# Performance work log

Hardware: AMD Instinct MI355X
Metric: run time of the kernel (lower is better)

## Reference

```python
import jax, jax.numpy as jnp
import numpy as np

B, T, D, H = 1024, 64, 256, 256  # batch, time steps, input_size, hidden_size


def setup_inputs() -> dict:
    key = jax.random.key(0)
    ks = jax.random.split(key, 5)
    s = 0.05
    return {
        "input_data": jax.random.normal(ks[0], (B, T, D), jnp.float32),
        # nn.Linear(2H+T, 1)
        "W_attn": jax.random.normal(ks[1], (1, 2 * H + T), jnp.float32) * s,
        "b_attn": jnp.zeros((1,), jnp.float32),
        # nn.LSTM(input_size=D, hidden_size=H, num_layers=1); gate order i,f,g,o
        "W_ih": jax.random.normal(ks[2], (4 * H, D), jnp.float32) * s,
        "W_hh": jax.random.normal(ks[3], (4 * H, H), jnp.float32) * s,
        "b_ih": jnp.zeros((4 * H,), jnp.float32),
        "b_hh": jnp.zeros((4 * H,), jnp.float32),
    }


def _encoder(input_data, W_attn, b_attn, W_ih, W_hh, b_ih, b_hh):
    Bv, Tv, Dv = input_data.shape
    Hv = W_hh.shape[1]
    # attn_linear applied to concat([h, c, x_series]) decomposes exactly into
    # three dot products (same math, no giant concat materialized each step).
    w_h = W_attn[0, :Hv]            # (H,)  weight on hidden part
    w_c = W_attn[0, Hv:2 * Hv]      # (H,)  weight on cell part
    w_x = W_attn[0, 2 * Hv:]        # (T,)  weight on per-feature time series
    # input_data.permute(0,2,1) @ w_x is constant across steps -> precompute.
    x_score = jnp.einsum('btd,t->bd', input_data, w_x) + b_attn[0]  # (B, D)

    xs = jnp.moveaxis(input_data, 1, 0)  # (T, B, D)

    def step(carry, x_t):
        h, c = carry                              # each (B, H)
        s_hc = h @ w_h + c @ w_c                  # (B,) same across features
        attn = jax.nn.softmax(s_hc[:, None] + x_score, axis=1)  # (B, D)
        w_in = attn * x_t                         # weighted input, (B, D)
        gates = w_in @ W_ih.T + h @ W_hh.T + b_ih + b_hh  # (B, 4H)
        i, f, g, o = jnp.split(gates, 4, axis=1)
        c_new = jax.nn.sigmoid(f) * c + jax.nn.sigmoid(i) * jnp.tanh(g)
        h_new = jax.nn.sigmoid(o) * jnp.tanh(c_new)
        return (h_new, c_new), (w_in, h_new)

    h0 = jnp.zeros((Bv, Hv), input_data.dtype)
    c0 = jnp.zeros((Bv, Hv), input_data.dtype)
    _, (ws, hs) = jax.lax.scan(step, (h0, c0), xs)
    input_weighted = jnp.moveaxis(ws, 0, 1)  # (B, T, D)
    input_encoded = jnp.moveaxis(hs, 0, 1)   # (B, T, H)
    return input_weighted, input_encoded


def reference(input_data, W_attn, b_attn, W_ih, W_hh, b_ih, b_hh):
    return _encoder(input_data, W_attn, b_attn, W_ih, W_hh, b_ih, b_hh)
```

## Files before the change

kernel.cpp:

```cpp
#include <hip/hip_runtime.h>
#include <hip/hip_bf16.h>
#include <stdint.h>

#define B_ 1024
#define T_ 64
#define D_ 256
#define H_ 256
#define G_ 1024

typedef float f32x4 __attribute__((ext_vector_type(4)));
typedef __bf16 bf16x8 __attribute__((ext_vector_type(8)));
typedef unsigned int u32x4 __attribute__((ext_vector_type(4)));

#if __has_builtin(__builtin_amdgcn_rcpf)
#define RCP(x) __builtin_amdgcn_rcpf(x)
#else
#define RCP(x) (1.f / (x))
#endif

__device__ __forceinline__ float bf2f(unsigned int u) {
    unsigned int x = u << 16;
    return __builtin_bit_cast(float, x);
}
__device__ __forceinline__ unsigned short f2bf(float f) {
    __hip_bfloat16 h = __float2bfloat16(f);
    return __builtin_bit_cast(unsigned short, h);
}

__global__ void prep_w_kernel(const float* __restrict__ Wih, const float* __restrict__ Whh,
                              const float* __restrict__ bih, const float* __restrict__ bhh,
                              unsigned short* __restrict__ wih_bf, unsigned short* __restrict__ whh_bf,
                              float* __restrict__ bias) {
    int i = blockIdx.x * 256 + threadIdx.x;
    wih_bf[i] = f2bf(Wih[i]);
    whh_bf[i] = f2bf(Whh[i]);
    if (i < G_) bias[i] = bih[i] + bhh[i];
}

__global__ void prep_attn_kernel(const float* __restrict__ x, const float* __restrict__ Wattn,
                                 float* __restrict__ attn) {
    __shared__ float wx[T_];
    __shared__ float red[256];
    int b = blockIdx.x, d = threadIdx.x;
    if (d < T_) wx[d] = Wattn[2 * H_ + d];
    __syncthreads();
    const float* xb = x + (size_t)b * T_ * D_ + d;
    float s = 0.f;
    #pragma unroll
    for (int t = 0; t < T_; ++t) s += xb[t * D_] * wx[t];
    red[d] = s;
    __syncthreads();
    for (int o = 128; o > 0; o >>= 1) {
        if (d < o) red[d] = fmaxf(red[d], red[d + o]);
        __syncthreads();
    }
    float m = red[0];
    __syncthreads();
    float e = __expf(s - m);
    red[d] = e;
    __syncthreads();
    for (int o = 128; o > 0; o >>= 1) {
        if (d < o) red[d] += red[d + o];
        __syncthreads();
    }
    attn[b * D_ + d] = e * (1.f / red[0]);
}

__global__ void winw_kernel(const float* __restrict__ x, const float* __restrict__ attn,
                            float* __restrict__ w_out, unsigned short* __restrict__ win_bf) {
    int i4 = blockIdx.x * 256 + threadIdx.x;
    int e  = i4 * 4;
    int d  = e & 255;
    int bt = e >> 8;
    int b  = bt >> 6, t = bt & 63;
    f32x4 xv = *(const f32x4*)(x + e);
    f32x4 av = *(const f32x4*)(attn + b * D_ + d);
    f32x4 w  = xv * av;
    *(f32x4*)(w_out + e) = w;
    ushort4 u;
    u.x = f2bf(w[0]); u.y = f2bf(w[1]); u.z = f2bf(w[2]); u.w = f2bf(w[3]);
    *(ushort4*)(win_bf + ((size_t)(t * B_ + b) * D_ + d)) = u;
}

__global__ __launch_bounds__(256, 2) void gemmx_kernel(const unsigned short* __restrict__ A,
                                                       const unsigned short* __restrict__ Bw,
                                                       unsigned short* __restrict__ pre) {
    int bx = blockIdx.x;
    int bn = bx & 7, bm = bx >> 3;
    int tid = threadIdx.x, lane = tid & 63, w = tid >> 6;
    int wr = w >> 1, wc = w & 1;
    int m0 = bm * 128 + wr * 64, n0 = bn * 128 + wc * 64;
    int lr = lane & 15, lk = (lane >> 4) * 8;

    const unsigned short* Ab[4];
    const unsigned short* Bb[4];
    #pragma unroll
    for (int i = 0; i < 4; ++i) {
        Ab[i] = A  + (size_t)(m0 + i * 16 + lr) * D_ + lk;
        Bb[i] = Bw + (size_t)(n0 + i * 16 + lr) * D_ + lk;
    }
    f32x4 acc[4][4] = {};
    #pragma unroll
    for (int kk = 0; kk < 8; ++kk) {
        bf16x8 a[4], bb[4];
        #pragma unroll
        for (int i = 0; i < 4; ++i) {
            a[i]  = *(const bf16x8*)(Ab[i] + kk * 32);
            bb[i] = *(const bf16x8*)(Bb[i] + kk * 32);
        }
        #pragma unroll
        for (int mi = 0; mi < 4; ++mi)
            #pragma unroll
            for (int ni = 0; ni < 4; ++ni)
                acc[mi][ni] = __builtin_amdgcn_mfma_f32_16x16x32_bf16(a[mi], bb[ni], acc[mi][ni], 0, 0, 0);
    }
    int orow = (lane >> 4) * 4;
    #pragma unroll
    for (int mi = 0; mi < 4; ++mi)
        #pragma unroll
        for (int ni = 0; ni < 4; ++ni)
            #pragma unroll
            for (int q = 0; q < 4; ++q) {
                int m = m0 + mi * 16 + orow + q;
                int n = n0 + ni * 16 + lr;
                pre[(size_t)m * G_ + n] = f2bf(acc[mi][ni][q]);
            }
}

__global__ __launch_bounds__(512, 2) void seqs_kernel(const unsigned short* __restrict__ pre,
                                                      const unsigned short* __restrict__ Whh,
                                                      const float* __restrict__ bias,
                                                      float* __restrict__ enc_out) {
    extern __shared__ char smem[];
    unsigned short* W_lds    = (unsigned short*)smem;
    unsigned short* h_par    = (unsigned short*)(smem + 135168);
    float*          bias_lds = (float*)(smem + 135168 + 16896);

    int tid = threadIdx.x, lane = tid & 63, w = tid >> 6;
    int lr = lane & 15, hi = lane >> 4;
    int r0 = blockIdx.x * 16;
    int j0 = w * 32;

    for (int i = tid; i < 1024; i += 512) bias_lds[i] = bias[i];
    for (int i = tid; i < 2 * 16 * 264; i += 512) h_par[i] = 0;
    #pragma unroll
    for (int l = 0; l < 2; ++l) {
        int n = l * 256 + j0 + 16 + lr;
        const u32x4* src = (const u32x4*)(Whh + (size_t)n * 256);
        #pragma unroll
        for (int c = 0; c < 8; ++c) {
            int ch = hi + c * 4;
            *(u32x4*)&W_lds[((w * 2 + l) * 16 + lr) * 264 + ch * 8] = src[ch];
        }
    }
    bf16x8 Wreg[4][8];
    #pragma unroll
    for (int g = 0; g < 4; ++g)
        #pragma unroll
        for (int kk = 0; kk < 8; ++kk)
            Wreg[g][kk] = *(const bf16x8*)(Whh + (size_t)(g * 256 + j0 + lr) * 256 + kk * 32 + hi * 8);
    const unsigned short* Ws[2];
    #pragma unroll
    for (int s = 0; s < 2; ++s)
        Ws[s] = Whh + (size_t)((s + 2) * 256 + j0 + 16 + lr) * 256 + hi * 8;
    bf16x8 sbuf[2][4];
    #pragma unroll
    for (int s = 0; s < 2; ++s)
        #pragma unroll
        for (int k2 = 0; k2 < 4; ++k2)
            sbuf[s][k2] = *(const bf16x8*)(Ws[s] + k2 * 32);

    const unsigned short* pbase = pre + (size_t)(r0 + hi * 4) * G_ + j0 + lr;
    float biasA[4], biasB[4];
    float cA[4] = {}, cB[4] = {};
    __syncthreads();
    #pragma unroll
    for (int g = 0; g < 4; ++g) {
        biasA[g] = bias_lds[g * 256 + j0 + lr];
        biasB[g] = bias_lds[g * 256 + j0 + 16 + lr];
    }

    #pragma unroll 1
    for (int t = 0; t < T_; ++t) {
        const unsigned short* Ps = pbase + (size_t)t * (1024u * 1024u);
        unsigned short curA[4][4], curB[4][4];
        #pragma unroll
        for (int g = 0; g < 4; ++g)
            #pragma unroll
            for (int q = 0; q < 4; ++q) {
                curA[g][q] = Ps[(size_t)q * 1024 + g * 256];
                curB[g][q] = Ps[(size_t)q * 1024 + g * 256 + 16];
            }

        int p = t & 1;
        const unsigned short* hrd = h_par + p * (16 * 264);
        unsigned short*       hwr = h_par + (p ^ 1) * (16 * 264);

        f32x4 acc[4] = {};
        #pragma unroll
        for (int kk = 0; kk < 8; ++kk) {
            bf16x8 a = *(const bf16x8*)&hrd[lr * 264 + kk * 32 + hi * 8];
            #pragma unroll
            for (int g = 0; g < 4; ++g)
                acc[g] = __builtin_amdgcn_mfma_f32_16x16x32_bf16(a, Wreg[g][kk], acc[g], 0, 0, 0);
        }
        #pragma unroll
        for (int q = 0; q < 4; ++q) {
            float gi = acc[0][q] + bf2f((unsigned)curA[0][q]) + biasA[0];
            float gf = acc[1][q] + bf2f((unsigned)curA[1][q]) + biasA[1];
            float gg = acc[2][q] + bf2f((unsigned)curA[2][q]) + biasA[2];
            float go = acc[3][q] + bf2f((unsigned)curA[3][q]) + biasA[3];
            float si = RCP(1.f + __expf(-gi));
            float sf = RCP(1.f + __expf(-gf));
            float so = RCP(1.f + __expf(-go));
            float tg = 1.f - 2.f * RCP(__expf(2.f * gg) + 1.f);
            float cn = sf * cA[q] + si * tg;
            cA[q] = cn;
            float tc = 1.f - 2.f * RCP(__expf(2.f * cn) + 1.f);
            float h  = so * tc;
            hwr[(hi * 4 + q) * 264 + j0 + lr] = f2bf(h);
            enc_out[((size_t)(r0 + hi * 4 + q) * T_ + t) * H_ + j0 + lr] = h;
        }

        f32x4 accB[4] = {};
        #pragma unroll
        for (int kk = 0; kk < 4; ++kk) {
            bf16x8 a  = *(const bf16x8*)&hrd[lr * 264 + kk * 32 + hi * 8];
            bf16x8 b0 = *(const bf16x8*)&W_lds[((w * 2 + 0) * 16 + lr) * 264 + kk * 32 + hi * 8];
            bf16x8 b1 = *(const bf16x8*)&W_lds[((w * 2 + 1) * 16 + lr) * 264 + kk * 32 + hi * 8];
            accB[0] = __builtin_amdgcn_mfma_f32_16x16x32_bf16(a, b0, accB[0], 0, 0, 0);
            accB[1] = __builtin_amdgcn_mfma_f32_16x16x32_bf16(a, b1, accB[1], 0, 0, 0);
            accB[2] = __builtin_amdgcn_mfma_f32_16x16x32_bf16(a, sbuf[0][kk], accB[2], 0, 0, 0);
            accB[3] = __builtin_amdgcn_mfma_f32_16x16x32_bf16(a, sbuf[1][kk], accB[3], 0, 0, 0);
        }
        #pragma unroll
        for (int s = 0; s < 2; ++s)
            #pragma unroll
            for (int k2 = 0; k2 < 4; ++k2)
                sbuf[s][k2] = *(const bf16x8*)(Ws[s] + (k2 + 4) * 32);
        #pragma unroll
        for (int kk = 4; kk < 8; ++kk) {
            bf16x8 a  = *(const bf16x8*)&hrd[lr * 264 + kk * 32 + hi * 8];
            bf16x8 b0 = *(const bf16x8*)&W_lds[((w * 2 + 0) * 16 + lr) * 264 + kk * 32 + hi * 8];
            bf16x8 b1 = *(const bf16x8*)&W_lds[((w * 2 + 1) * 16 + lr) * 264 + kk * 32 + hi * 8];
            accB[0] = __builtin_amdgcn_mfma_f32_16x16x32_bf16(a, b0, accB[0], 0, 0, 0);
            accB[1] = __builtin_amdgcn_mfma_f32_16x16x32_bf16(a, b1, accB[1], 0, 0, 0);
            accB[2] = __builtin_amdgcn_mfma_f32_16x16x32_bf16(a, sbuf[0][kk - 4], accB[2], 0, 0, 0);
            accB[3] = __builtin_amdgcn_mfma_f32_16x16x32_bf16(a, sbuf[1][kk - 4], accB[3], 0, 0, 0);
        }
        #pragma unroll
        for (int s = 0; s < 2; ++s)
            #pragma unroll
            for (int k2 = 0; k2 < 4; ++k2)
                sbuf[s][k2] = *(const bf16x8*)(Ws[s] + k2 * 32);

        #pragma unroll
        for (int q = 0; q < 4; ++q) {
            float gi = accB[0][q] + bf2f((unsigned)curB[0][q]) + biasB[0];
            float gf = accB[1][q] + bf2f((unsigned)curB[1][q]) + biasB[1];
            float gg = accB[2][q] + bf2f((unsigned)curB[2][q]) + biasB[2];
            float go = accB[3][q] + bf2f((unsigned)curB[3][q]) + biasB[3];
            float si = RCP(1.f + __expf(-gi));
            float sf = RCP(1.f + __expf(-gf));
            float so = RCP(1.f + __expf(-go));
            float tg = 1.f - 2.f * RCP(__expf(2.f * gg) + 1.f);
            float cn = sf * cB[q] + si * tg;
            cB[q] = cn;
            float tc = 1.f - 2.f * RCP(__expf(2.f * cn) + 1.f);
            float h  = so * tc;
            hwr[(hi * 4 + q) * 264 + j0 + 16 + lr] = f2bf(h);
            enc_out[((size_t)(r0 + hi * 4 + q) * T_ + t) * H_ + j0 + 16 + lr] = h;
        }

        asm volatile("s_waitcnt lgkmcnt(0)" ::: "memory");
        __builtin_amdgcn_s_barrier();
    }
}

extern "C" void kernel_launch(void* const* d_in, const int* in_sizes, int n_in,
                              void* d_out, int out_size, void* d_ws, size_t ws_size,
                              hipStream_t stream) {
    const float* x     = (const float*)d_in[0];
    const float* Wattn = (const float*)d_in[1];
    const float* Wih   = (const float*)d_in[3];
    const float* Whh   = (const float*)d_in[4];
    const float* bih   = (const float*)d_in[5];
    const float* bhh   = (const float*)d_in[6];

    char* ws = (char*)d_ws;
    float*          attn   = (float*)(ws);
    unsigned short* win_bf = (unsigned short*)(ws + 1048576);
    unsigned short* wih_bf = (unsigned short*)(ws + 34603008);
    unsigned short* whh_bf = (unsigned short*)(ws + 35127296);
    float*          bias   = (float*)(ws + 35651584);
    unsigned short* pre    = (unsigned short*)(ws + 35659776);

    float* w_out   = (float*)d_out;
    float* enc_out = (float*)d_out + (size_t)B_ * T_ * D_;

    hipFuncSetAttribute((const void*)seqs_kernel,
                        hipFuncAttributeMaxDynamicSharedMemorySize, 156160);

    prep_w_kernel<<<dim3(1024), dim3(256), 0, stream>>>(Wih, Whh, bih, bhh, wih_bf, whh_bf, bias);
    prep_attn_kernel<<<dim3(1024), dim3(256), 0, stream>>>(x, Wattn, attn);
    winw_kernel<<<dim3(16384), dim3(256), 0, stream>>>(x, attn, w_out, win_bf);
    gemmx_kernel<<<dim3(4096), dim3(256), 0, stream>>>(win_bf, wih_bf, pre);
    seqs_kernel<<<dim3(64), dim3(512), 156160, stream>>>(pre, whh_bf, bias, enc_out);
}
```

Baseline: 459.6 us.

## Store recurrent weights and hidden state in MFMA fragment order in LDS

Rearranges the LDS copies of the W_hh slice and the hidden-state double buffer into per-lane MFMA fragment order, so each lane reads its operand with one contiguous 16-byte access instead of a padded row-major stride. Hidden-state writes pair neighbouring bf16 values with a lane shuffle and store them as dwords. Bias now comes straight from global memory into registers rather than through LDS, and the second-half pre-activation loads move after the first MFMA block. It also pins the register-resident weights with asm barriers, adds a sched_barrier after the step barrier, and shrinks the LDS allocation; the extra shuffles and changed scheduling could add latency on the serial critical path.

```diff
diff --git a/kernel.cpp b/kernel.cpp
--- a/kernel.cpp
+++ b/kernel.cpp
@@ -127,38 +127,44 @@
             }
 }
 
-__global__ __launch_bounds__(512, 2) void seqs_kernel(const unsigned short* __restrict__ pre,
-                                                      const unsigned short* __restrict__ Whh,
-                                                      const float* __restrict__ bias,
-                                                      float* __restrict__ enc_out) {
+__global__ __launch_bounds__(512)
+__attribute__((amdgpu_waves_per_eu(2, 2)))
+void seqs_kernel(const unsigned short* __restrict__ pre,
+                 const unsigned short* __restrict__ Whh,
+                 const float* __restrict__ bias,
+                 float* __restrict__ enc_out) {
     extern __shared__ char smem[];
-    unsigned short* W_lds    = (unsigned short*)smem;
-    unsigned short* h_par    = (unsigned short*)(smem + 135168);
-    float*          bias_lds = (float*)(smem + 135168 + 16896);
+    unsigned short* W_frag = (unsigned short*)smem;
+    unsigned short* h_frag = (unsigned short*)(smem + 131072);
 
     int tid = threadIdx.x, lane = tid & 63, w = tid >> 6;
     int lr = lane & 15, hi = lane >> 4;
     int r0 = blockIdx.x * 16;
     int j0 = w * 32;
 
-    for (int i = tid; i < 1024; i += 512) bias_lds[i] = bias[i];
-    for (int i = tid; i < 2 * 16 * 264; i += 512) h_par[i] = 0;
     #pragma unroll
     for (int l = 0; l < 2; ++l) {
         int n = l * 256 + j0 + 16 + lr;
-        const u32x4* src = (const u32x4*)(Whh + (size_t)n * 256);
-        #pragma unroll
-        for (int c = 0; c < 8; ++c) {
-            int ch = hi + c * 4;
-            *(u32x4*)&W_lds[((w * 2 + l) * 16 + lr) * 264 + ch * 8] = src[ch];
-        }
-    }
+        const unsigned short* src = Whh + (size_t)n * 256 + hi * 8;
+        #pragma unroll
+        for (int c = 0; c < 8; ++c)
+            *(u32x4*)&W_frag[(((w * 2 + l) * 8 + c) * 64 + lane) * 8] =
+                *(const u32x4*)(src + c * 32);
+    }
+    for (int i = tid; i < 4096; i += 512) ((unsigned int*)h_frag)[i] = 0;
+
     bf16x8 Wreg[4][8];
     #pragma unroll
     for (int g = 0; g < 4; ++g)
         #pragma unroll
         for (int kk = 0; kk < 8; ++kk)
             Wreg[g][kk] = *(const bf16x8*)(Whh + (size_t)(g * 256 + j0 + lr) * 256 + kk * 32 + hi * 8);
+    #pragma unroll
+    for (int g = 0; g < 4; ++g)
+        #pragma unroll
+        for (int kk = 0; kk < 8; ++kk)
+            asm volatile("" : "+v"(Wreg[g][kk]));
+
     const unsigned short* Ws[2];
     #pragma unroll
     for (int s = 0; s < 2; ++s)
@@ -172,38 +178,45 @@
 
     const unsigned short* pbase = pre + (size_t)(r0 + hi * 4) * G_ + j0 + lr;
     float biasA[4], biasB[4];
+    #pragma unroll
+    for (int g = 0; g < 4; ++g) {
+        biasA[g] = bias[g * 256 + j0 + lr];
+        biasB[g] = bias[g * 256 + j0 + 16 + lr];
+    }
     float cA[4] = {}, cB[4] = {};
-    __syncthreads();
-    #pragma unroll
-    for (int g = 0; g < 4; ++g) {
-        biasA[g] = bias_lds[g * 256 + j0 + lr];
-        biasB[g] = bias_lds[g * 256 + j0 + 16 + lr];
-    }
+
+    __syncthreads();
 
     #pragma unroll 1
     for (int t = 0; t < T_; ++t) {
         const unsigned short* Ps = pbase + (size_t)t * (1024u * 1024u);
-        unsigned short curA[4][4], curB[4][4];
+        unsigned short curA[4][4];
         #pragma unroll
         for (int g = 0; g < 4; ++g)
             #pragma unroll
-            for (int q = 0; q < 4; ++q) {
+            for (int q = 0; q < 4; ++q)
                 curA[g][q] = Ps[(size_t)q * 1024 + g * 256];
-                curB[g][q] = Ps[(size_t)q * 1024 + g * 256 + 16];
-            }
 
         int p = t & 1;
-        const unsigned short* hrd = h_par + p * (16 * 264);
-        unsigned short*       hwr = h_par + (p ^ 1) * (16 * 264);
+        const unsigned short* hrd = h_frag + p * 4096;
+        unsigned short*       hwr = h_frag + (p ^ 1) * 4096;
 
         f32x4 acc[4] = {};
         #pragma unroll
         for (int kk = 0; kk < 8; ++kk) {
-            bf16x8 a = *(const bf16x8*)&hrd[lr * 264 + kk * 32 + hi * 8];
+            bf16x8 a = *(const bf16x8*)&hrd[(kk * 64 + lane) * 8];
             #pragma unroll
             for (int g = 0; g < 4; ++g)
                 acc[g] = __builtin_amdgcn_mfma_f32_16x16x32_bf16(a, Wreg[g][kk], acc[g], 0, 0, 0);
         }
+
+        unsigned short curB[4][4];
+        #pragma unroll
+        for (int g = 0; g < 4; ++g)
+            #pragma unroll
+            for (int q = 0; q < 4; ++q)
+                curB[g][q] = Ps[(size_t)q * 1024 + g * 256 + 16];
+
         #pragma unroll
         for (int q = 0; q < 4; ++q) {
             float gi = acc[0][q] + bf2f((unsigned)curA[0][q]) + biasA[0];
@@ -218,16 +231,21 @@
             cA[q] = cn;
             float tc = 1.f - 2.f * RCP(__expf(2.f * cn) + 1.f);
             float h  = so * tc;
-            hwr[(hi * 4 + q) * 264 + j0 + lr] = f2bf(h);
+            unsigned int hu = (unsigned int)f2bf(h);
+            unsigned int ph = (unsigned int)__shfl_xor((int)hu, 1);
+            if ((lr & 1) == 0) {
+                unsigned int dw = hu | (ph << 16);
+                *(unsigned int*)&hwr[w * 512 + (((lr >> 3) * 16) + hi * 4 + q) * 8 + (lr & 7)] = dw;
+            }
             enc_out[((size_t)(r0 + hi * 4 + q) * T_ + t) * H_ + j0 + lr] = h;
         }
 
         f32x4 accB[4] = {};
         #pragma unroll
         for (int kk = 0; kk < 4; ++kk) {
-            bf16x8 a  = *(const bf16x8*)&hrd[lr * 264 + kk * 32 + hi * 8];
-            bf16x8 b0 = *(const bf16x8*)&W_lds[((w * 2 + 0) * 16 + lr) * 264 + kk * 32 + hi * 8];
-            bf16x8 b1 = *(const bf16x8*)&W_lds[((w * 2 + 1) * 16 + lr) * 264 + kk * 32 + hi * 8];
+            bf16x8 a  = *(const bf16x8*)&hrd[(kk * 64 + lane) * 8];
+            bf16x8 b0 = *(const bf16x8*)&W_frag[(((w * 2 + 0) * 8 + kk) * 64 + lane) * 8];
+            bf16x8 b1 = *(const bf16x8*)&W_frag[(((w * 2 + 1) * 8 + kk) * 64 + lane) * 8];
             accB[0] = __builtin_amdgcn_mfma_f32_16x16x32_bf16(a, b0, accB[0], 0, 0, 0);
             accB[1] = __builtin_amdgcn_mfma_f32_16x16x32_bf16(a, b1, accB[1], 0, 0, 0);
             accB[2] = __builtin_amdgcn_mfma_f32_16x16x32_bf16(a, sbuf[0][kk], accB[2], 0, 0, 0);
@@ -240,9 +258,9 @@
                 sbuf[s][k2] = *(const bf16x8*)(Ws[s] + (k2 + 4) * 32);
         #pragma unroll
         for (int kk = 4; kk < 8; ++kk) {
-            bf16x8 a  = *(const bf16x8*)&hrd[lr * 264 + kk * 32 + hi * 8];
-            bf16x8 b0 = *(const bf16x8*)&W_lds[((w * 2 + 0) * 16 + lr) * 264 + kk * 32 + hi * 8];
-            bf16x8 b1 = *(const bf16x8*)&W_lds[((w * 2 + 1) * 16 + lr) * 264 + kk * 32 + hi * 8];
+            bf16x8 a  = *(const bf16x8*)&hrd[(kk * 64 + lane) * 8];
+            bf16x8 b0 = *(const bf16x8*)&W_frag[(((w * 2 + 0) * 8 + kk) * 64 + lane) * 8];
+            bf16x8 b1 = *(const bf16x8*)&W_frag[(((w * 2 + 1) * 8 + kk) * 64 + lane) * 8];
             accB[0] = __builtin_amdgcn_mfma_f32_16x16x32_bf16(a, b0, accB[0], 0, 0, 0);
             accB[1] = __builtin_amdgcn_mfma_f32_16x16x32_bf16(a, b1, accB[1], 0, 0, 0);
             accB[2] = __builtin_amdgcn_mfma_f32_16x16x32_bf16(a, sbuf[0][kk - 4], accB[2], 0, 0, 0);
@@ -268,12 +286,18 @@
             cB[q] = cn;
             float tc = 1.f - 2.f * RCP(__expf(2.f * cn) + 1.f);
             float h  = so * tc;
-            hwr[(hi * 4 + q) * 264 + j0 + 16 + lr] = f2bf(h);
+            unsigned int hu = (unsigned int)f2bf(h);
+            unsigned int ph = (unsigned int)__shfl_xor((int)hu, 1);
+            if ((lr & 1) == 0) {
+                unsigned int dw = hu | (ph << 16);
+                *(unsigned int*)&hwr[w * 512 + ((32 + (lr >> 3) * 16) + hi * 4 + q) * 8 + (lr & 7)] = dw;
+            }
             enc_out[((size_t)(r0 + hi * 4 + q) * T_ + t) * H_ + j0 + 16 + lr] = h;
         }
 
         asm volatile("s_waitcnt lgkmcnt(0)" ::: "memory");
         __builtin_amdgcn_s_barrier();
+        __builtin_amdgcn_sched_barrier(0);
     }
 }
 
@@ -299,11 +323,11 @@
     float* enc_out = (float*)d_out + (size_t)B_ * T_ * D_;
 
     hipFuncSetAttribute((const void*)seqs_kernel,
-                        hipFuncAttributeMaxDynamicSharedMemorySize, 156160);
+                        hipFuncAttributeMaxDynamicSharedMemorySize, 147456);
 
     prep_w_kernel<<<dim3(1024), dim3(256), 0, stream>>>(Wih, Whh, bih, bhh, wih_bf, whh_bf, bias);
     prep_attn_kernel<<<dim3(1024), dim3(256), 0, stream>>>(x, Wattn, attn);
     winw_kernel<<<dim3(16384), dim3(256), 0, stream>>>(x, attn, w_out, win_bf);
     gemmx_kernel<<<dim3(4096), dim3(256), 0, stream>>>(win_bf, wih_bf, pre);
-    seqs_kernel<<<dim3(64), dim3(512), 156160, stream>>>(pre, whh_bf, bias, enc_out);
-}
+    seqs_kernel<<<dim3(64), dim3(512), 147456, stream>>>(pre, whh_bf, bias, enc_out);
+}
```

New measurement: 475.6 us. +3.5%, slower.
